# Kernel optimization log

Hardware: AMD Instinct MI355X
Metric: run time of the kernel (lower is better)

## Reference

```python
import jax, jax.numpy as jnp
import numpy as np

N, L, D = 512, 40, 128      # batch, peptide length, embedding dim
O, K, MHC = 256, 9, 34      # out_channels, kernel_size, mhc_len
STRIDE = 1


def setup_inputs() -> dict:
    key = jax.random.key(0)
    k1, k2, k3 = jax.random.split(key, 3)
    peptide_x = jax.random.normal(k1, (N, L, D), dtype=jnp.float32)
    mhc_x = jax.random.normal(k2, (N, MHC, D), dtype=jnp.float32)
    weight = jax.random.normal(k3, (O, K, MHC), dtype=jnp.float32) * 0.02  # truncated_normal std=0.02 approx
    bias = jnp.zeros((O,), dtype=jnp.float32)
    return {"peptide_x": peptide_x, "mhc_x": mhc_x, "weight": weight, "bias": bias}


def reference(peptide_x, mhc_x, weight, bias):
    # Per-sample dynamic kernel generation: [n, O, d, K]
    kernel = jax.nn.relu(jnp.einsum('nld,okl->nodk', mhc_x, weight))
    k = weight.shape[1]
    T = (peptide_x.shape[1] - k) // STRIDE + 1  # conv1d output length
    # Sliding windows of the peptide: [n, T, K, d]
    idx = jnp.arange(T)[:, None] * STRIDE + jnp.arange(k)[None, :]
    win = peptide_x[:, idx, :]
    # Grouped (groups=batch) conv1d as a batched contraction: [n, O, T]
    out = jnp.einsum('ntkd,nodk->not', win, kernel) + bias[None, :, None]
    return out
```

## Files before the change

kernel.cpp:

```cpp
#include <hip/hip_runtime.h>
#include <hip/hip_bf16.h>

typedef unsigned short u16;
typedef unsigned int u32;
typedef __bf16 bf16x8 __attribute__((ext_vector_type(8)));
typedef float f32x4 __attribute__((ext_vector_type(4)));
typedef unsigned int u32x4 __attribute__((ext_vector_type(4)));
typedef unsigned int u32x2 __attribute__((ext_vector_type(2)));

#define NN 512
#define LL 40
#define DD 128
#define OO 256
#define KK 9
#define MHCL 34
#define TT 32
#define PSTR 136
#define KDSTR 72
#define WPADL 64

#define PEPT_U16 (LL * PSTR)
#define KS_U16   (32 * KDSTR)

__device__ __forceinline__ u16 f2bf(float x) {
    unsigned int u = __builtin_bit_cast(unsigned int, x);
    u = (u + 0x7FFFu + ((u >> 16) & 1u)) >> 16;
    return (u16)u;
}
__device__ __forceinline__ u32 pk2(float a, float b) {
    __hip_bfloat162 h = __float22bfloat162_rn(make_float2(a, b));
    u32 r;
    __builtin_memcpy(&r, &h, 4);
    return r;
}
__device__ __forceinline__ bf16x8 ld8(const u16* p) {
    u32x4 r;
    __builtin_memcpy(&r, __builtin_assume_aligned(p, 16), 16);
    return __builtin_bit_cast(bf16x8, r);
}
__device__ __forceinline__ f32x4 mfma16(bf16x8 a, bf16x8 b, f32x4 c) {
    return __builtin_amdgcn_mfma_f32_16x16x32_bf16(a, b, c, 0, 0, 0);
}

__global__ void w_convert(const float* __restrict__ wgt, u32* __restrict__ wp) {
    int i = blockIdx.x * 256 + threadIdx.x;
    if (i >= OO * KK * (WPADL / 2)) return;
    int o = i / (KK * (WPADL / 2));
    int r = i - o * (KK * (WPADL / 2));
    int k = r >> 5;
    int lp = (r & 31) << 1;
    const float* src = wgt + ((size_t)o * KK + k) * MHCL;
    float a = (lp     < MHCL) ? src[lp]     : 0.f;
    float b = (lp + 1 < MHCL) ? src[lp + 1] : 0.f;
    wp[i] = pk2(a, b);
}

__global__ void p_convert(const float* __restrict__ pept, u32* __restrict__ pp) {
    size_t i = (size_t)blockIdx.x * 256 + threadIdx.x;
    if (i >= (size_t)NN * LL * DD / 2) return;
    pp[i] = pk2(pept[2 * i], pept[2 * i + 1]);
}

__global__ __launch_bounds__(256, 2)
void iconv_fast(const float* __restrict__ mhc,
                const u16* __restrict__ wp,
                const u16* __restrict__ pb,
                const float* __restrict__ bias,
                float* __restrict__ out)
{
    __shared__ __align__(16) u16 s_mem[PEPT_U16 + 4 * KS_U16];

    const int tid  = threadIdx.x;
    const int wave = tid >> 6;
    const int pair = wave >> 1;
    const int dh   = wave & 1;
    const int lane = tid & 63;
    const int quad = lane >> 4;
    const int l16  = lane & 15;

    const int n  = blockIdx.x >> 2;
    const int oq = blockIdx.x & 3;
    const int obase = (oq * 2 + pair) * 32;

    u16* const s_pept = s_mem;
    u16* const ks     = s_mem + PEPT_U16 + wave * KS_U16;

    auto loadW = [&](int o_base, int k, bf16x8 wF[2][2]) {
        #pragma unroll
        for (int mt = 0; mt < 2; ++mt) {
            const u16* wr = wp + ((size_t)(o_base + mt * 16 + l16) * KK + k) * WPADL;
            u32x4 r0, r1;
            __builtin_memcpy(&r0, __builtin_assume_aligned(wr + quad * 8, 16), 16);
            __builtin_memcpy(&r1, __builtin_assume_aligned(wr + 32 + quad * 8, 16), 16);
            wF[mt][0] = __builtin_bit_cast(bf16x8, r0);
            wF[mt][1] = __builtin_bit_cast(bf16x8, r1);
        }
    };

    bf16x8 wB[2][2];
    loadW(obase, 0, wB);

    bf16x8 mA[4][2];
    {
        const float* mg = mhc + (size_t)n * MHCL * DD;
        #pragma unroll
        for (int di = 0; di < 4; ++di) {
            const int d = dh * 64 + di * 16 + l16;
            u16 h0[8];
            #pragma unroll
            for (int j = 0; j < 8; ++j)
                h0[j] = f2bf(mg[(size_t)(quad * 8 + j) * DD + d]);
            __builtin_memcpy(&mA[di][0], h0, 16);
            u16 h1[8] = {0,0,0,0,0,0,0,0};
            if (quad == 0) {
                h1[0] = f2bf(mg[(size_t)32 * DD + d]);
                h1[1] = f2bf(mg[(size_t)33 * DD + d]);
            }
            __builtin_memcpy(&mA[di][1], h1, 16);
        }
    }

    {
        const u16* pg = pb + (size_t)n * LL * DD;
        #pragma unroll 1
        for (int i = tid; i < (LL * DD) / 8; i += 256) {
            int row = i >> 4, c8 = (i & 15) << 3;
            u32x4 v;
            __builtin_memcpy(&v, __builtin_assume_aligned(pg + (size_t)row * DD + c8, 16), 16);
            __builtin_memcpy(__builtin_assume_aligned(&s_pept[row * PSTR + c8], 16), &v, 16);
        }
    }
    __syncthreads();

    f32x4 acc00 = {0.f,0.f,0.f,0.f}, acc01 = acc00, acc10 = acc00, acc11 = acc00;

    #pragma unroll 3
    for (int k = 0; k < KK; ++k) {
        #pragma unroll
        for (int di = 0; di < 4; ++di) {
            f32x4 c0 = {0.f,0.f,0.f,0.f}, c1 = c0;
            c0 = mfma16(mA[di][0], wB[0][0], c0);
            c0 = mfma16(mA[di][1], wB[0][1], c0);
            c1 = mfma16(mA[di][0], wB[1][0], c1);
            c1 = mfma16(mA[di][1], wB[1][1], c1);
            u32x2 p0 = { pk2(fmaxf(c0[0], 0.f), fmaxf(c0[1], 0.f)),
                         pk2(fmaxf(c0[2], 0.f), fmaxf(c0[3], 0.f)) };
            u32x2 p1 = { pk2(fmaxf(c1[0], 0.f), fmaxf(c1[1], 0.f)),
                         pk2(fmaxf(c1[2], 0.f), fmaxf(c1[3], 0.f)) };
            __builtin_memcpy(__builtin_assume_aligned(&ks[l16 * KDSTR + di * 16 + quad * 4], 8), &p0, 8);
            __builtin_memcpy(__builtin_assume_aligned(&ks[(16 + l16) * KDSTR + di * 16 + quad * 4], 8), &p1, 8);
        }
        if (k < KK - 1) loadW(obase, k + 1, wB);
        #pragma unroll
        for (int ds = 0; ds < 2; ++ds) {
            bf16x8 kb0 = ld8(&ks[l16 * KDSTR + ds * 32 + quad * 8]);
            bf16x8 kb1 = ld8(&ks[(16 + l16) * KDSTR + ds * 32 + quad * 8]);
            bf16x8 ap0 = ld8(&s_pept[(k + l16) * PSTR + dh * 64 + ds * 32 + quad * 8]);
            bf16x8 ap1 = ld8(&s_pept[(k + 16 + l16) * PSTR + dh * 64 + ds * 32 + quad * 8]);
            acc00 = mfma16(ap0, kb0, acc00);
            acc01 = mfma16(ap0, kb1, acc01);
            acc10 = mfma16(ap1, kb0, acc10);
            acc11 = mfma16(ap1, kb1, acc11);
        }
    }

    if (dh == 1) {
        float* ox = (float*)ks;
        const int fb = lane * 16;
        __builtin_memcpy(__builtin_assume_aligned(&ox[fb +  0], 16), &acc00, 16);
        __builtin_memcpy(__builtin_assume_aligned(&ox[fb +  4], 16), &acc01, 16);
        __builtin_memcpy(__builtin_assume_aligned(&ox[fb +  8], 16), &acc10, 16);
        __builtin_memcpy(__builtin_assume_aligned(&ox[fb + 12], 16), &acc11, 16);
    }
    __syncthreads();
    if (dh == 0) {
        const float* px = (const float*)(s_mem + PEPT_U16 + (wave + 1) * KS_U16);
        const int fb = lane * 16;
        f32x4 q00, q01, q10, q11;
        __builtin_memcpy(&q00, __builtin_assume_aligned(&px[fb +  0], 16), 16);
        __builtin_memcpy(&q01, __builtin_assume_aligned(&px[fb +  4], 16), 16);
        __builtin_memcpy(&q10, __builtin_assume_aligned(&px[fb +  8], 16), 16);
        __builtin_memcpy(&q11, __builtin_assume_aligned(&px[fb + 12], 16), 16);
        const float bv0 = bias[obase + l16];
        const float bv1 = bias[obase + 16 + l16];
        f32x4 r00 = acc00 + q00 + bv0;
        f32x4 r01 = acc01 + q01 + bv1;
        f32x4 r10 = acc10 + q10 + bv0;
        f32x4 r11 = acc11 + q11 + bv1;
        float* ob = out + ((size_t)n * OO + obase) * TT;
        __builtin_memcpy(__builtin_assume_aligned(ob + (size_t)l16 * TT + quad * 4, 16), &r00, 16);
        __builtin_memcpy(__builtin_assume_aligned(ob + (size_t)(16 + l16) * TT + quad * 4, 16), &r01, 16);
        __builtin_memcpy(__builtin_assume_aligned(ob + (size_t)l16 * TT + 16 + quad * 4, 16), &r10, 16);
        __builtin_memcpy(__builtin_assume_aligned(ob + (size_t)(16 + l16) * TT + 16 + quad * 4, 16), &r11, 16);
    }
}

__global__ __launch_bounds__(256, 2)
void iconv_ref(const float* __restrict__ pept,
               const float* __restrict__ mhc,
               const float* __restrict__ wgt,
               const float* __restrict__ bias,
               float* __restrict__ out)
{
    __shared__ __align__(16) u16 s_mem[PEPT_U16 + 4 * KS_U16];
    const int tid  = threadIdx.x;
    const int wave = tid >> 6;
    const int pair = wave >> 1;
    const int dh   = wave & 1;
    const int lane = tid & 63;
    const int quad = lane >> 4;
    const int l16  = lane & 15;
    const int n  = blockIdx.x >> 2;
    const int oq = blockIdx.x & 3;
    const int obase = (oq * 2 + pair) * 32;
    u16* const s_pept = s_mem;
    u16* const ks     = s_mem + PEPT_U16 + wave * KS_U16;

    auto loadW = [&](int o_base, int k, bf16x8 wF[2][2]) {
        #pragma unroll
        for (int mt = 0; mt < 2; ++mt) {
            const float* wrow = wgt + ((size_t)(o_base + mt * 16 + l16) * KK + k) * MHCL;
            float w8[8];
            __builtin_memcpy(w8, __builtin_assume_aligned(wrow + quad * 8, 8), 32);
            u16 h0[8];
            #pragma unroll
            for (int j = 0; j < 8; ++j) h0[j] = f2bf(w8[j]);
            __builtin_memcpy(&wF[mt][0], h0, 16);
            u16 h1[8] = {0,0,0,0,0,0,0,0};
            if (quad == 0) { h1[0] = f2bf(wrow[32]); h1[1] = f2bf(wrow[33]); }
            __builtin_memcpy(&wF[mt][1], h1, 16);
        }
    };

    bf16x8 wB[2][2];
    loadW(obase, 0, wB);

    bf16x8 mA[4][2];
    {
        const float* mg = mhc + (size_t)n * MHCL * DD;
        #pragma unroll
        for (int di = 0; di < 4; ++di) {
            const int d = dh * 64 + di * 16 + l16;
            u16 h0[8];
            #pragma unroll
            for (int j = 0; j < 8; ++j)
                h0[j] = f2bf(mg[(size_t)(quad * 8 + j) * DD + d]);
            __builtin_memcpy(&mA[di][0], h0, 16);
            u16 h1[8] = {0,0,0,0,0,0,0,0};
            if (quad == 0) {
                h1[0] = f2bf(mg[(size_t)32 * DD + d]);
                h1[1] = f2bf(mg[(size_t)33 * DD + d]);
            }
            __builtin_memcpy(&mA[di][1], h1, 16);
        }
    }

    {
        const float* pg = pept + (size_t)n * LL * DD;
        #pragma unroll 1
        for (int i = tid; i < (LL * DD) / 4; i += 256) {
            int row = i >> 5, c4 = (i & 31) << 2;
            f32x4 v;
            __builtin_memcpy(&v, __builtin_assume_aligned(pg + row * DD + c4, 16), 16);
            u32x2 h = { pk2(v[0], v[1]), pk2(v[2], v[3]) };
            __builtin_memcpy(__builtin_assume_aligned(&s_pept[row * PSTR + c4], 8), &h, 8);
        }
    }
    __syncthreads();

    f32x4 acc00 = {0.f,0.f,0.f,0.f}, acc01 = acc00, acc10 = acc00, acc11 = acc00;

    #pragma unroll 3
    for (int k = 0; k < KK; ++k) {
        #pragma unroll
        for (int di = 0; di < 4; ++di) {
            f32x4 c0 = {0.f,0.f,0.f,0.f}, c1 = c0;
            c0 = mfma16(mA[di][0], wB[0][0], c0);
            c0 = mfma16(mA[di][1], wB[0][1], c0);
            c1 = mfma16(mA[di][0], wB[1][0], c1);
            c1 = mfma16(mA[di][1], wB[1][1], c1);
            u32x2 p0 = { pk2(fmaxf(c0[0], 0.f), fmaxf(c0[1], 0.f)),
                         pk2(fmaxf(c0[2], 0.f), fmaxf(c0[3], 0.f)) };
            u32x2 p1 = { pk2(fmaxf(c1[0], 0.f), fmaxf(c1[1], 0.f)),
                         pk2(fmaxf(c1[2], 0.f), fmaxf(c1[3], 0.f)) };
            __builtin_memcpy(__builtin_assume_aligned(&ks[l16 * KDSTR + di * 16 + quad * 4], 8), &p0, 8);
            __builtin_memcpy(__builtin_assume_aligned(&ks[(16 + l16) * KDSTR + di * 16 + quad * 4], 8), &p1, 8);
        }
        if (k < KK - 1) loadW(obase, k + 1, wB);
        #pragma unroll
        for (int ds = 0; ds < 2; ++ds) {
            bf16x8 kb0 = ld8(&ks[l16 * KDSTR + ds * 32 + quad * 8]);
            bf16x8 kb1 = ld8(&ks[(16 + l16) * KDSTR + ds * 32 + quad * 8]);
            bf16x8 ap0 = ld8(&s_pept[(k + l16) * PSTR + dh * 64 + ds * 32 + quad * 8]);
            bf16x8 ap1 = ld8(&s_pept[(k + 16 + l16) * PSTR + dh * 64 + ds * 32 + quad * 8]);
            acc00 = mfma16(ap0, kb0, acc00);
            acc01 = mfma16(ap0, kb1, acc01);
            acc10 = mfma16(ap1, kb0, acc10);
            acc11 = mfma16(ap1, kb1, acc11);
        }
    }

    if (dh == 1) {
        float* ox = (float*)ks;
        const int fb = lane * 16;
        __builtin_memcpy(__builtin_assume_aligned(&ox[fb +  0], 16), &acc00, 16);
        __builtin_memcpy(__builtin_assume_aligned(&ox[fb +  4], 16), &acc01, 16);
        __builtin_memcpy(__builtin_assume_aligned(&ox[fb +  8], 16), &acc10, 16);
        __builtin_memcpy(__builtin_assume_aligned(&ox[fb + 12], 16), &acc11, 16);
    }
    __syncthreads();
    if (dh == 0) {
        const float* px = (const float*)(s_mem + PEPT_U16 + (wave + 1) * KS_U16);
        const int fb = lane * 16;
        f32x4 q00, q01, q10, q11;
        __builtin_memcpy(&q00, __builtin_assume_aligned(&px[fb +  0], 16), 16);
        __builtin_memcpy(&q01, __builtin_assume_aligned(&px[fb +  4], 16), 16);
        __builtin_memcpy(&q10, __builtin_assume_aligned(&px[fb +  8], 16), 16);
        __builtin_memcpy(&q11, __builtin_assume_aligned(&px[fb + 12], 16), 16);
        const float bv0 = bias[obase + l16];
        const float bv1 = bias[obase + 16 + l16];
        f32x4 r00 = acc00 + q00 + bv0;
        f32x4 r01 = acc01 + q01 + bv1;
        f32x4 r10 = acc10 + q10 + bv0;
        f32x4 r11 = acc11 + q11 + bv1;
        float* ob = out + ((size_t)n * OO + obase) * TT;
        __builtin_memcpy(__builtin_assume_aligned(ob + (size_t)l16 * TT + quad * 4, 16), &r00, 16);
        __builtin_memcpy(__builtin_assume_aligned(ob + (size_t)(16 + l16) * TT + quad * 4, 16), &r01, 16);
        __builtin_memcpy(__builtin_assume_aligned(ob + (size_t)l16 * TT + 16 + quad * 4, 16), &r10, 16);
        __builtin_memcpy(__builtin_assume_aligned(ob + (size_t)(16 + l16) * TT + 16 + quad * 4, 16), &r11, 16);
    }
}

extern "C" void kernel_launch(void* const* d_in, const int* in_sizes, int n_in,
                              void* d_out, int out_size, void* d_ws, size_t ws_size,
                              hipStream_t stream) {
    const float* pept = (const float*)d_in[0];
    const float* mhc  = (const float*)d_in[1];
    const float* wgt  = (const float*)d_in[2];
    const float* bias = (const float*)d_in[3];
    float* out = (float*)d_out;

    const size_t w_bytes = (size_t)OO * KK * WPADL * sizeof(u16);
    const size_t p_bytes = (size_t)NN * LL * DD * sizeof(u16);
    if (ws_size >= w_bytes + p_bytes) {
        u16* wp = (u16*)d_ws;
        u16* pp = (u16*)((char*)d_ws + w_bytes);
        w_convert<<<dim3((OO * KK * (WPADL / 2) + 255) / 256), dim3(256), 0, stream>>>(wgt, (u32*)wp);
        p_convert<<<dim3((NN * LL * DD / 2 + 255) / 256), dim3(256), 0, stream>>>(pept, (u32*)pp);
        iconv_fast<<<dim3(NN * 4), dim3(256), 0, stream>>>(mhc, wp, pp, bias, out);
    } else {
        iconv_ref<<<dim3(NN * 4), dim3(256), 0, stream>>>(pept, mhc, wgt, bias, out);
    }
}
```

Before: 119.0 us.

## Keep generated kernel in registers via permuted d-mapping and merge conversion kernels

The MHC operand's d index is permuted so the MFMA output fragments of the per-sample kernel line up with the B-operand layout of the second MFMA. The relu'd bf16 kernel values can then be repacked in registers instead of stored to and reloaded from LDS. This shrinks shared memory to a small exchange buffer, which may also help occupancy. Separately, the weight and peptide bf16 conversion kernels are merged into one launch to save a kernel launch.

```diff
diff --git a/kernel.cpp b/kernel.cpp
--- a/kernel.cpp
+++ b/kernel.cpp
@@ -21,6 +21,7 @@
 
 #define PEPT_U16 (LL * PSTR)
 #define KS_U16   (32 * KDSTR)
+#define EX_U16   2048
 
 __device__ __forceinline__ u16 f2bf(float x) {
     unsigned int u = __builtin_bit_cast(unsigned int, x);
@@ -42,23 +43,24 @@
     return __builtin_amdgcn_mfma_f32_16x16x32_bf16(a, b, c, 0, 0, 0);
 }
 
-__global__ void w_convert(const float* __restrict__ wgt, u32* __restrict__ wp) {
+__global__ void cvt_all(const float* __restrict__ wgt, const float* __restrict__ pept,
+                        u32* __restrict__ wp, u32* __restrict__ pp) {
     int i = blockIdx.x * 256 + threadIdx.x;
-    if (i >= OO * KK * (WPADL / 2)) return;
-    int o = i / (KK * (WPADL / 2));
-    int r = i - o * (KK * (WPADL / 2));
-    int k = r >> 5;
-    int lp = (r & 31) << 1;
-    const float* src = wgt + ((size_t)o * KK + k) * MHCL;
-    float a = (lp     < MHCL) ? src[lp]     : 0.f;
-    float b = (lp + 1 < MHCL) ? src[lp + 1] : 0.f;
-    wp[i] = pk2(a, b);
-}
-
-__global__ void p_convert(const float* __restrict__ pept, u32* __restrict__ pp) {
-    size_t i = (size_t)blockIdx.x * 256 + threadIdx.x;
-    if (i >= (size_t)NN * LL * DD / 2) return;
-    pp[i] = pk2(pept[2 * i], pept[2 * i + 1]);
+    const int WN = OO * KK * (WPADL / 2);
+    if (i < WN) {
+        int o = i / (KK * (WPADL / 2));
+        int r = i - o * (KK * (WPADL / 2));
+        int k = r >> 5;
+        int lp = (r & 31) << 1;
+        const float* src = wgt + ((size_t)o * KK + k) * MHCL;
+        float a = (lp     < MHCL) ? src[lp]     : 0.f;
+        float b = (lp + 1 < MHCL) ? src[lp + 1] : 0.f;
+        wp[i] = pk2(a, b);
+    } else {
+        size_t j = (size_t)(i - WN);
+        if (j < (size_t)NN * LL * DD / 2)
+            pp[j] = pk2(pept[2 * j], pept[2 * j + 1]);
+    }
 }
 
 __global__ __launch_bounds__(256, 2)
@@ -68,7 +70,7 @@
                 const float* __restrict__ bias,
                 float* __restrict__ out)
 {
-    __shared__ __align__(16) u16 s_mem[PEPT_U16 + 4 * KS_U16];
+    __shared__ __align__(16) u16 s_mem[PEPT_U16 + 2 * EX_U16];
 
     const int tid  = threadIdx.x;
     const int wave = tid >> 6;
@@ -83,7 +85,6 @@
     const int obase = (oq * 2 + pair) * 32;
 
     u16* const s_pept = s_mem;
-    u16* const ks     = s_mem + PEPT_U16 + wave * KS_U16;
 
     auto loadW = [&](int o_base, int k, bf16x8 wF[2][2]) {
         #pragma unroll
@@ -94,6 +95,141 @@
             __builtin_memcpy(&r1, __builtin_assume_aligned(wr + 32 + quad * 8, 16), 16);
             wF[mt][0] = __builtin_bit_cast(bf16x8, r0);
             wF[mt][1] = __builtin_bit_cast(bf16x8, r1);
+        }
+    };
+
+    bf16x8 wB[2][2];
+    loadW(obase, 0, wB);
+
+    bf16x8 mA[4][2];
+    {
+        const float* mg = mhc + (size_t)n * MHCL * DD;
+        #pragma unroll
+        for (int di = 0; di < 4; ++di) {
+            const int d = dh * 64 + 32 * (di & 1) + 8 * (l16 >> 2) + 4 * (di >> 1) + (l16 & 3);
+            u16 h0[8];
+            #pragma unroll
+            for (int j = 0; j < 8; ++j)
+                h0[j] = f2bf(mg[(size_t)(quad * 8 + j) * DD + d]);
+            __builtin_memcpy(&mA[di][0], h0, 16);
+            u16 h1[8] = {0,0,0,0,0,0,0,0};
+            if (quad == 0) {
+                h1[0] = f2bf(mg[(size_t)32 * DD + d]);
+                h1[1] = f2bf(mg[(size_t)33 * DD + d]);
+            }
+            __builtin_memcpy(&mA[di][1], h1, 16);
+        }
+    }
+
+    {
+        const u16* pg = pb + (size_t)n * LL * DD;
+        #pragma unroll 1
+        for (int i = tid; i < (LL * DD) / 8; i += 256) {
+            int row = i >> 4, c8 = (i & 15) << 3;
+            u32x4 v;
+            __builtin_memcpy(&v, __builtin_assume_aligned(pg + (size_t)row * DD + c8, 16), 16);
+            __builtin_memcpy(__builtin_assume_aligned(&s_pept[row * PSTR + c8], 16), &v, 16);
+        }
+    }
+    __syncthreads();
+
+    f32x4 acc00 = {0.f,0.f,0.f,0.f}, acc01 = acc00, acc10 = acc00, acc11 = acc00;
+
+    #pragma unroll 3
+    for (int k = 0; k < KK; ++k) {
+        u32x2 kc0[4], kc1[4];
+        #pragma unroll
+        for (int di = 0; di < 4; ++di) {
+            f32x4 c0 = {0.f,0.f,0.f,0.f}, c1 = c0;
+            c0 = mfma16(mA[di][0], wB[0][0], c0);
+            c0 = mfma16(mA[di][1], wB[0][1], c0);
+            c1 = mfma16(mA[di][0], wB[1][0], c1);
+            c1 = mfma16(mA[di][1], wB[1][1], c1);
+            kc0[di][0] = pk2(fmaxf(c0[0], 0.f), fmaxf(c0[1], 0.f));
+            kc0[di][1] = pk2(fmaxf(c0[2], 0.f), fmaxf(c0[3], 0.f));
+            kc1[di][0] = pk2(fmaxf(c1[0], 0.f), fmaxf(c1[1], 0.f));
+            kc1[di][1] = pk2(fmaxf(c1[2], 0.f), fmaxf(c1[3], 0.f));
+        }
+        if (k < KK - 1) loadW(obase, k + 1, wB);
+        #pragma unroll
+        for (int ds = 0; ds < 2; ++ds) {
+            u32x4 b0 = { kc0[ds][0], kc0[ds][1], kc0[ds + 2][0], kc0[ds + 2][1] };
+            u32x4 b1 = { kc1[ds][0], kc1[ds][1], kc1[ds + 2][0], kc1[ds + 2][1] };
+            bf16x8 bk0 = __builtin_bit_cast(bf16x8, b0);
+            bf16x8 bk1 = __builtin_bit_cast(bf16x8, b1);
+            bf16x8 ap0 = ld8(&s_pept[(k + l16) * PSTR + dh * 64 + ds * 32 + quad * 8]);
+            bf16x8 ap1 = ld8(&s_pept[(k + 16 + l16) * PSTR + dh * 64 + ds * 32 + quad * 8]);
+            acc00 = mfma16(ap0, bk0, acc00);
+            acc01 = mfma16(ap0, bk1, acc01);
+            acc10 = mfma16(ap1, bk0, acc10);
+            acc11 = mfma16(ap1, bk1, acc11);
+        }
+    }
+
+    if (dh == 1) {
+        float* ox = (float*)(s_mem + PEPT_U16 + pair * EX_U16);
+        const int fb = lane * 16;
+        __builtin_memcpy(__builtin_assume_aligned(&ox[fb +  0], 16), &acc00, 16);
+        __builtin_memcpy(__builtin_assume_aligned(&ox[fb +  4], 16), &acc01, 16);
+        __builtin_memcpy(__builtin_assume_aligned(&ox[fb +  8], 16), &acc10, 16);
+        __builtin_memcpy(__builtin_assume_aligned(&ox[fb + 12], 16), &acc11, 16);
+    }
+    __syncthreads();
+    if (dh == 0) {
+        const float* px = (const float*)(s_mem + PEPT_U16 + pair * EX_U16);
+        const int fb = lane * 16;
+        f32x4 q00, q01, q10, q11;
+        __builtin_memcpy(&q00, __builtin_assume_aligned(&px[fb +  0], 16), 16);
+        __builtin_memcpy(&q01, __builtin_assume_aligned(&px[fb +  4], 16), 16);
+        __builtin_memcpy(&q10, __builtin_assume_aligned(&px[fb +  8], 16), 16);
+        __builtin_memcpy(&q11, __builtin_assume_aligned(&px[fb + 12], 16), 16);
+        const float bv0 = bias[obase + l16];
+        const float bv1 = bias[obase + 16 + l16];
+        f32x4 r00 = acc00 + q00 + bv0;
+        f32x4 r01 = acc01 + q01 + bv1;
+        f32x4 r10 = acc10 + q10 + bv0;
+        f32x4 r11 = acc11 + q11 + bv1;
+        float* ob = out + ((size_t)n * OO + obase) * TT;
+        __builtin_memcpy(__builtin_assume_aligned(ob + (size_t)l16 * TT + quad * 4, 16), &r00, 16);
+        __builtin_memcpy(__builtin_assume_aligned(ob + (size_t)(16 + l16) * TT + quad * 4, 16), &r01, 16);
+        __builtin_memcpy(__builtin_assume_aligned(ob + (size_t)l16 * TT + 16 + quad * 4, 16), &r10, 16);
+        __builtin_memcpy(__builtin_assume_aligned(ob + (size_t)(16 + l16) * TT + 16 + quad * 4, 16), &r11, 16);
+    }
+}
+
+__global__ __launch_bounds__(256, 2)
+void iconv_ref(const float* __restrict__ pept,
+               const float* __restrict__ mhc,
+               const float* __restrict__ wgt,
+               const float* __restrict__ bias,
+               float* __restrict__ out)
+{
+    __shared__ __align__(16) u16 s_mem[PEPT_U16 + 4 * KS_U16];
+    const int tid  = threadIdx.x;
+    const int wave = tid >> 6;
+    const int dh   = wave & 1;
+    const int lane = tid & 63;
+    const int quad = lane >> 4;
+    const int l16  = lane & 15;
+    const int n  = blockIdx.x >> 2;
+    const int oq = blockIdx.x & 3;
+    const int obase = (oq * 2 + (wave >> 1)) * 32;
+    u16* const s_pept = s_mem;
+    u16* const ks     = s_mem + PEPT_U16 + wave * KS_U16;
+
+    auto loadW = [&](int o_base, int k, bf16x8 wF[2][2]) {
+        #pragma unroll
+        for (int mt = 0; mt < 2; ++mt) {
+            const float* wrow = wgt + ((size_t)(o_base + mt * 16 + l16) * KK + k) * MHCL;
+            float w8[8];
+            __builtin_memcpy(w8, __builtin_assume_aligned(wrow + quad * 8, 8), 32);
+            u16 h0[8];
+            #pragma unroll
+            for (int j = 0; j < 8; ++j) h0[j] = f2bf(w8[j]);
+            __builtin_memcpy(&wF[mt][0], h0, 16);
+            u16 h1[8] = {0,0,0,0,0,0,0,0};
+            if (quad == 0) { h1[0] = f2bf(wrow[32]); h1[1] = f2bf(wrow[33]); }
+            __builtin_memcpy(&wF[mt][1], h1, 16);
         }
     };
 
@@ -121,13 +257,14 @@
     }
 
     {
-        const u16* pg = pb + (size_t)n * LL * DD;
+        const float* pg = pept + (size_t)n * LL * DD;
         #pragma unroll 1
-        for (int i = tid; i < (LL * DD) / 8; i += 256) {
-            int row = i >> 4, c8 = (i & 15) << 3;
-            u32x4 v;
-            __builtin_memcpy(&v, __builtin_assume_aligned(pg + (size_t)row * DD + c8, 16), 16);
-            __builtin_memcpy(__builtin_assume_aligned(&s_pept[row * PSTR + c8], 16), &v, 16);
+        for (int i = tid; i < (LL * DD) / 4; i += 256) {
+            int row = i >> 5, c4 = (i & 31) << 2;
+            f32x4 v;
+            __builtin_memcpy(&v, __builtin_assume_aligned(pg + row * DD + c4, 16), 16);
+            u32x2 h = { pk2(v[0], v[1]), pk2(v[2], v[3]) };
+            __builtin_memcpy(__builtin_assume_aligned(&s_pept[row * PSTR + c4], 8), &h, 8);
         }
     }
     __syncthreads();
@@ -195,142 +332,6 @@
     }
 }
 
-__global__ __launch_bounds__(256, 2)
-void iconv_ref(const float* __restrict__ pept,
-               const float* __restrict__ mhc,
-               const float* __restrict__ wgt,
-               const float* __restrict__ bias,
-               float* __restrict__ out)
-{
-    __shared__ __align__(16) u16 s_mem[PEPT_U16 + 4 * KS_U16];
-    const int tid  = threadIdx.x;
-    const int wave = tid >> 6;
-    const int pair = wave >> 1;
-    const int dh   = wave & 1;
-    const int lane = tid & 63;
-    const int quad = lane >> 4;
-    const int l16  = lane & 15;
-    const int n  = blockIdx.x >> 2;
-    const int oq = blockIdx.x & 3;
-    const int obase = (oq * 2 + pair) * 32;
-    u16* const s_pept = s_mem;
-    u16* const ks     = s_mem + PEPT_U16 + wave * KS_U16;
-
-    auto loadW = [&](int o_base, int k, bf16x8 wF[2][2]) {
-        #pragma unroll
-        for (int mt = 0; mt < 2; ++mt) {
-            const float* wrow = wgt + ((size_t)(o_base + mt * 16 + l16) * KK + k) * MHCL;
-            float w8[8];
-            __builtin_memcpy(w8, __builtin_assume_aligned(wrow + quad * 8, 8), 32);
-            u16 h0[8];
-            #pragma unroll
-            for (int j = 0; j < 8; ++j) h0[j] = f2bf(w8[j]);
-            __builtin_memcpy(&wF[mt][0], h0, 16);
-            u16 h1[8] = {0,0,0,0,0,0,0,0};
-            if (quad == 0) { h1[0] = f2bf(wrow[32]); h1[1] = f2bf(wrow[33]); }
-            __builtin_memcpy(&wF[mt][1], h1, 16);
-        }
-    };
-
-    bf16x8 wB[2][2];
-    loadW(obase, 0, wB);
-
-    bf16x8 mA[4][2];
-    {
-        const float* mg = mhc + (size_t)n * MHCL * DD;
-        #pragma unroll
-        for (int di = 0; di < 4; ++di) {
-            const int d = dh * 64 + di * 16 + l16;
-            u16 h0[8];
-            #pragma unroll
-            for (int j = 0; j < 8; ++j)
-                h0[j] = f2bf(mg[(size_t)(quad * 8 + j) * DD + d]);
-            __builtin_memcpy(&mA[di][0], h0, 16);
-            u16 h1[8] = {0,0,0,0,0,0,0,0};
-            if (quad == 0) {
-                h1[0] = f2bf(mg[(size_t)32 * DD + d]);
-                h1[1] = f2bf(mg[(size_t)33 * DD + d]);
-            }
-            __builtin_memcpy(&mA[di][1], h1, 16);
-        }
-    }
-
-    {
-        const float* pg = pept + (size_t)n * LL * DD;
-        #pragma unroll 1
-        for (int i = tid; i < (LL * DD) / 4; i += 256) {
-            int row = i >> 5, c4 = (i & 31) << 2;
-            f32x4 v;
-            __builtin_memcpy(&v, __builtin_assume_aligned(pg + row * DD + c4, 16), 16);
-            u32x2 h = { pk2(v[0], v[1]), pk2(v[2], v[3]) };
-            __builtin_memcpy(__builtin_assume_aligned(&s_pept[row * PSTR + c4], 8), &h, 8);
-        }
-    }
-    __syncthreads();
-
-    f32x4 acc00 = {0.f,0.f,0.f,0.f}, acc01 = acc00, acc10 = acc00, acc11 = acc00;
-
-    #pragma unroll 3
-    for (int k = 0; k < KK; ++k) {
-        #pragma unroll
-        for (int di = 0; di < 4; ++di) {
-            f32x4 c0 = {0.f,0.f,0.f,0.f}, c1 = c0;
-            c0 = mfma16(mA[di][0], wB[0][0], c0);
-            c0 = mfma16(mA[di][1], wB[0][1], c0);
-            c1 = mfma16(mA[di][0], wB[1][0], c1);
-            c1 = mfma16(mA[di][1], wB[1][1], c1);
-            u32x2 p0 = { pk2(fmaxf(c0[0], 0.f), fmaxf(c0[1], 0.f)),
-                         pk2(fmaxf(c0[2], 0.f), fmaxf(c0[3], 0.f)) };
-            u32x2 p1 = { pk2(fmaxf(c1[0], 0.f), fmaxf(c1[1], 0.f)),
-                         pk2(fmaxf(c1[2], 0.f), fmaxf(c1[3], 0.f)) };
-            __builtin_memcpy(__builtin_assume_aligned(&ks[l16 * KDSTR + di * 16 + quad * 4], 8), &p0, 8);
-            __builtin_memcpy(__builtin_assume_aligned(&ks[(16 + l16) * KDSTR + di * 16 + quad * 4], 8), &p1, 8);
-        }
-        if (k < KK - 1) loadW(obase, k + 1, wB);
-        #pragma unroll
-        for (int ds = 0; ds < 2; ++ds) {
-            bf16x8 kb0 = ld8(&ks[l16 * KDSTR + ds * 32 + quad * 8]);
-            bf16x8 kb1 = ld8(&ks[(16 + l16) * KDSTR + ds * 32 + quad * 8]);
-            bf16x8 ap0 = ld8(&s_pept[(k + l16) * PSTR + dh * 64 + ds * 32 + quad * 8]);
-            bf16x8 ap1 = ld8(&s_pept[(k + 16 + l16) * PSTR + dh * 64 + ds * 32 + quad * 8]);
-            acc00 = mfma16(ap0, kb0, acc00);
-            acc01 = mfma16(ap0, kb1, acc01);
-            acc10 = mfma16(ap1, kb0, acc10);
-            acc11 = mfma16(ap1, kb1, acc11);
-        }
-    }
-
-    if (dh == 1) {
-        float* ox = (float*)ks;
-        const int fb = lane * 16;
-        __builtin_memcpy(__builtin_assume_aligned(&ox[fb +  0], 16), &acc00, 16);
-        __builtin_memcpy(__builtin_assume_aligned(&ox[fb +  4], 16), &acc01, 16);
-        __builtin_memcpy(__builtin_assume_aligned(&ox[fb +  8], 16), &acc10, 16);
-        __builtin_memcpy(__builtin_assume_aligned(&ox[fb + 12], 16), &acc11, 16);
-    }
-    __syncthreads();
-    if (dh == 0) {
-        const float* px = (const float*)(s_mem + PEPT_U16 + (wave + 1) * KS_U16);
-        const int fb = lane * 16;
-        f32x4 q00, q01, q10, q11;
-        __builtin_memcpy(&q00, __builtin_assume_aligned(&px[fb +  0], 16), 16);
-        __builtin_memcpy(&q01, __builtin_assume_aligned(&px[fb +  4], 16), 16);
-        __builtin_memcpy(&q10, __builtin_assume_aligned(&px[fb +  8], 16), 16);
-        __builtin_memcpy(&q11, __builtin_assume_aligned(&px[fb + 12], 16), 16);
-        const float bv0 = bias[obase + l16];
-        const float bv1 = bias[obase + 16 + l16];
-        f32x4 r00 = acc00 + q00 + bv0;
-        f32x4 r01 = acc01 + q01 + bv1;
-        f32x4 r10 = acc10 + q10 + bv0;
-        f32x4 r11 = acc11 + q11 + bv1;
-        float* ob = out + ((size_t)n * OO + obase) * TT;
-        __builtin_memcpy(__builtin_assume_aligned(ob + (size_t)l16 * TT + quad * 4, 16), &r00, 16);
-        __builtin_memcpy(__builtin_assume_aligned(ob + (size_t)(16 + l16) * TT + quad * 4, 16), &r01, 16);
-        __builtin_memcpy(__builtin_assume_aligned(ob + (size_t)l16 * TT + 16 + quad * 4, 16), &r10, 16);
-        __builtin_memcpy(__builtin_assume_aligned(ob + (size_t)(16 + l16) * TT + 16 + quad * 4, 16), &r11, 16);
-    }
-}
-
 extern "C" void kernel_launch(void* const* d_in, const int* in_sizes, int n_in,
                               void* d_out, int out_size, void* d_ws, size_t ws_size,
                               hipStream_t stream) {
@@ -345,8 +346,8 @@
     if (ws_size >= w_bytes + p_bytes) {
         u16* wp = (u16*)d_ws;
         u16* pp = (u16*)((char*)d_ws + w_bytes);
-        w_convert<<<dim3((OO * KK * (WPADL / 2) + 255) / 256), dim3(256), 0, stream>>>(wgt, (u32*)wp);
-        p_convert<<<dim3((NN * LL * DD / 2 + 255) / 256), dim3(256), 0, stream>>>(pept, (u32*)pp);
+        const int total = OO * KK * (WPADL / 2) + NN * LL * DD / 2;
+        cvt_all<<<dim3((total + 255) / 256), dim3(256), 0, stream>>>(wgt, pept, (u32*)wp, (u32*)pp);
         iconv_fast<<<dim3(NN * 4), dim3(256), 0, stream>>>(mhc, wp, pp, bias, out);
     } else {
         iconv_ref<<<dim3(NN * 4), dim3(256), 0, stream>>>(pept, mhc, wgt, bias, out);
```

Measured after the change: 116.7 us (median of 2 runs). Within noise of the previous version (-1.9%).
